# Optimization experiments

Hardware: AMD Instinct MI355X
Metric: run time of the kernel (lower is better)

## Reference

```python
import jax, jax.numpy as jnp
from jax import lax
import numpy as np

B, L, DIM = 4, 4096, 512
H, HD = 8, 64            # num_heads, head_dim
CHUNK = 128              # chunk size for chunk-recurrent lightning attention
LN_EPS = 1e-5


def _slopes(h):
    # _build_slope_tensor for power-of-2 heads: 2^(-8*(i+1)/h), cast through fp16
    s = np.array([2.0 ** (-8.0 * (i + 1) / h) for i in range(h)], dtype=np.float32)
    return jnp.asarray(s.astype(np.float16).astype(np.float32))  # [h]


def _layernorm(x, w, b):
    mu = jnp.mean(x, axis=-1, keepdims=True)
    var = jnp.mean((x - mu) ** 2, axis=-1, keepdims=True)
    return (x - mu) * lax.rsqrt(var + LN_EPS) * w + b


def _rmsnorm(x, gamma):
    # F.normalize(x, dim=-1) * sqrt(d) * gamma ; gamma [h,1,d] broadcasts over [b,h,l,d]
    n = x / jnp.maximum(jnp.linalg.norm(x, axis=-1, keepdims=True), 1e-12)
    return n * (HD ** 0.5) * gamma


def _lightning_attn(q, k, v, slopes):
    # q,k,v: [b,h,L,d]; causal linear attention with per-head decay exp(-s*(t-j))
    b, h, l, d = q.shape
    nc = l // CHUNK
    s = slopes[:, None, None]                      # [h,1,1]
    r = jnp.arange(CHUNK, dtype=q.dtype)
    diff = r[:, None] - r[None, :]                 # [C,C]
    Dintra = jnp.where(diff >= 0, jnp.exp(-s * diff), 0.0)   # [h,C,C]
    q_dec = jnp.exp(-slopes[:, None] * r[None, :])           # [h,C] decay from chunk start
    k_dec = jnp.exp(-slopes[:, None] * (CHUNK - r[None, :])) # [h,C] decay to next chunk start
    c_dec = jnp.exp(-slopes * CHUNK)                         # [h]

    def to_chunks(t):
        return t.reshape(b, h, nc, CHUNK, d).transpose(2, 0, 1, 3, 4)  # [nc,b,h,C,d]

    qc, kc, vc = to_chunks(q), to_chunks(k), to_chunks(v)

    def step(kv, inp):
        qi, ki, vi = inp                                       # [b,h,C,d]
        scores = jnp.einsum('bhid,bhjd->bhij', qi, ki) * Dintra[None]
        intra = jnp.einsum('bhij,bhjd->bhid', scores, vi)
        inter = jnp.einsum('bhcd,bhde->bhce', qi * q_dec[None, :, :, None], kv)
        kv = kv * c_dec[None, :, None, None] + jnp.einsum(
            'bhcd,bhce->bhde', ki * k_dec[None, :, :, None], vi)
        return kv, intra + inter

    kv0 = jnp.zeros((b, h, d, d), q.dtype)
    _, out = lax.scan(step, kv0, (qc, kc, vc))                 # [nc,b,h,C,d]
    return out.transpose(1, 2, 0, 3, 4).reshape(b, h, l, d)


def setup_inputs() -> dict:
    key = jax.random.key(0)
    ks = jax.random.split(key, 8)
    std = lambda fan_in: 1.0 / np.sqrt(fan_in)
    return {
        'x': jax.random.normal(ks[0], (B, L, DIM), jnp.float32),
        'ln1_w': jnp.ones((DIM,), jnp.float32),
        'ln1_b': jnp.zeros((DIM,), jnp.float32),
        'rel_bias': 0.02 * jax.random.normal(ks[1], (1, L, DIM), jnp.float32),
        'qkv_w': std(DIM) * jax.random.normal(ks[2], (3 * DIM, DIM), jnp.float32),
        'qkv_b': jnp.zeros((3 * DIM,), jnp.float32),
        'gq': jnp.ones((H, 1, HD), jnp.float32) / (HD ** 0.5),
        'gk': jnp.ones((H, 1, HD), jnp.float32) / (HD ** 0.5),
        'proj_w': std(DIM) * jax.random.normal(ks[3], (DIM, DIM), jnp.float32),
        'proj_b': jnp.zeros((DIM,), jnp.float32),
        'ln2_w': jnp.ones((DIM,), jnp.float32),
        'ln2_b': jnp.zeros((DIM,), jnp.float32),
        'fc1_w': std(DIM) * jax.random.normal(ks[4], (4 * DIM, DIM), jnp.float32),
        'fc1_b': jnp.zeros((4 * DIM,), jnp.float32),
        'fc2_w': std(4 * DIM) * jax.random.normal(ks[5], (DIM, 4 * DIM), jnp.float32),
        'fc2_b': jnp.zeros((DIM,), jnp.float32),
    }


def reference(x, ln1_w, ln1_b, rel_bias, qkv_w, qkv_b, gq, gk,
              proj_w, proj_b, ln2_w, ln2_b, fc1_w, fc1_b, fc2_w, fc2_b):
    slopes = _slopes(H)
    b, l, c = x.shape
    shortcut = x
    h = _layernorm(x, ln1_w, ln1_b)
    # --- LightningAttention ---
    h = h + rel_bias
    qkv = (h @ qkv_w.T + qkv_b).reshape(b, l, 3, H, HD).transpose(2, 0, 3, 1, 4)
    q, k, v = qkv[0], qkv[1], qkv[2]                     # [b,h,l,d]
    q = _rmsnorm(q * (HD ** -0.5), gq)
    k = _rmsnorm(k, gk)
    o = _lightning_attn(q, k, v, slopes)                 # [b,h,l,d]
    o = o.reshape(b, l, c)                               # faithful to source: reshape, no head transpose
    o = o @ proj_w.T + proj_b
    x = o + shortcut
    # --- MLP ---
    shortcut = x
    h = _layernorm(x, ln2_w, ln2_b)
    h = jax.nn.gelu(h @ fc1_w.T + fc1_b, approximate=False)
    h = h @ fc2_w.T + fc2_b
    return h + shortcut
```

## Files before the change

kernel.cpp:

```cpp
#include <hip/hip_runtime.h>
#include <math.h>

typedef unsigned short u16;
typedef __bf16 bf16x8 __attribute__((ext_vector_type(8)));
typedef float f32x4 __attribute__((ext_vector_type(4)));

#define DEVI static __device__ __forceinline__

DEVI float b2f(u16 u) { union { unsigned int i; float f; } w; w.i = ((unsigned int)u) << 16; return w.f; }
DEVI u16 f2b(float f) {
  union { float f; unsigned int i; } w; w.f = f;
  unsigned int r = (w.i + 0x7FFFu + ((w.i >> 16) & 1u)) >> 16;
  return (u16)r;
}
DEVI u16 cvt_bf16(float f) { __bf16 h = (__bf16)f; union { __bf16 h; u16 u; } w; w.h = h; return w.u; }

DEVI float fast_gelu(float v) {
  float x2 = v * v;
  float p = fmaf(0.10294357f, x2, 2.30215855f);
  float ex = exp2f(-v * p);
  return v * __builtin_amdgcn_rcpf(1.0f + ex);
}

__global__ void conv4_kernel(const float* __restrict__ s0, u16* __restrict__ d0, int n0,
                             const float* __restrict__ s1, u16* __restrict__ d1, int n1,
                             const float* __restrict__ s2, u16* __restrict__ d2, int n2,
                             const float* __restrict__ s3, u16* __restrict__ d3, int n3) {
  int i = blockIdx.x * 256 + threadIdx.x;
  int st = gridDim.x * 256;
  int tot = n0 + n1 + n2 + n3;
  for (; i < tot; i += st) {
    int j = i;
    if (j < n0) { d0[j] = f2b(s0[j]); continue; }
    j -= n0;
    if (j < n1) { d1[j] = f2b(s1[j]); continue; }
    j -= n1;
    if (j < n2) { d2[j] = f2b(s2[j]); continue; }
    j -= n2;
    d3[j] = f2b(s3[j]);
  }
}

template<int ADD_REL>
__global__ __launch_bounds__(256) void ln_kernel(
    const float* __restrict__ x, const float* __restrict__ w, const float* __restrict__ bb,
    const float* __restrict__ rel, u16* __restrict__ out) {
  int row = blockIdx.x;
  int t = threadIdx.x;
  const float* xr = x + (size_t)row * 512;
  float v0 = xr[t], v1 = xr[t + 256];
  float s = v0 + v1, ss = v0 * v0 + v1 * v1;
#pragma unroll
  for (int o = 32; o > 0; o >>= 1) { s += __shfl_down(s, o); ss += __shfl_down(ss, o); }
  __shared__ float rs[4], rss[4];
  int lane = t & 63, wid = t >> 6;
  if (lane == 0) { rs[wid] = s; rss[wid] = ss; }
  __syncthreads();
  s = rs[0] + rs[1] + rs[2] + rs[3];
  ss = rss[0] + rss[1] + rss[2] + rss[3];
  float mu = s * (1.0f / 512.0f);
  float inv = rsqrtf(ss * (1.0f / 512.0f) - mu * mu + 1e-5f);
  float o0 = (v0 - mu) * inv * w[t] + bb[t];
  float o1 = (v1 - mu) * inv * w[t + 256] + bb[t + 256];
  if (ADD_REL) {
    const float* rr = rel + (size_t)(row & 4095) * 512;
    o0 += rr[t]; o1 += rr[t + 256];
  }
  u16* orow = out + (size_t)row * 512;
  orow[t] = f2b(o0);
  orow[t + 256] = f2b(o1);
}

template<int EPI, int TM, int NSLOT>
__global__ __launch_bounds__(256) void gemm_bt_kernel(
    const u16* __restrict__ A, const u16* __restrict__ W,
    const float* __restrict__ bias, int M, int N, int K, int NBN,
    const float* __restrict__ resid, u16* __restrict__ outb,
    u16* __restrict__ q_out, u16* __restrict__ k_out, u16* __restrict__ v_out,
    float* __restrict__ outf, const float* __restrict__ gq, const float* __restrict__ gk) {
  constexpr int WM   = TM / 2;
  constexpr int NI   = TM / 32;
  constexpr int CA   = TM / 64;
  constexpr int SLOT = (TM + 128) * 32;
  __shared__ __align__(16) u16 sbuf[NSLOT * SLOT];
  int nwg = gridDim.x, wg = blockIdx.x;
  int wgs = (wg & 7) * (nwg >> 3) + (wg >> 3);
  int bn = wgs % NBN, bm = wgs / NBN;
  int m0 = bm * TM, n0 = bn * 128;
  int t = threadIdx.x, lane = t & 63, wid = t >> 6;
  int wrM = (wid >> 1) * WM, wc = (wid & 1) * 64;
  int fr = lane & 15, fq = lane >> 4;
  int srowA = wid * (TM / 4) + (lane >> 2);
  int srowB = wid * 32 + (lane >> 2);
  int scol = (((lane & 3) ^ ((lane >> 2) & 3))) * 8;
  const u16* gA = A + (size_t)(m0 + srowA) * K + scol;
  const u16* gB = W + (size_t)(n0 + srowB) * K + scol;
  f32x4 acc[NI][4] = {};
  auto AS = [&](int sel) { return &sbuf[sel * SLOT]; };
  auto BS = [&](int sel) { return &sbuf[sel * SLOT + TM * 32]; };
  auto STAGE = [&](int sel, int k0) {
    u16* lA = AS(sel) + wid * (CA * 512);
    u16* lB = BS(sel) + wid * 1024;
#pragma unroll
    for (int c = 0; c < CA; ++c)
      __builtin_amdgcn_global_load_lds(gA + k0 + c * 16 * K, lA + c * 512, 16, 0, 0);
    __builtin_amdgcn_global_load_lds(gB + k0,          lB,       16, 0, 0);
    __builtin_amdgcn_global_load_lds(gB + k0 + 16 * K, lB + 512, 16, 0, 0);
  };
  auto COMPUTE = [&](int sel) {
    bf16x8 af[NI], bfr[4];
#pragma unroll
    for (int i = 0; i < NI; ++i) {
      int ar = wrM + i * 16 + fr;
      af[i] = *(const bf16x8*)&AS(sel)[ar * 32 + ((fq ^ (ar & 3)) << 3)];
    }
#pragma unroll
    for (int j = 0; j < 4; ++j) {
      int br = wc + j * 16 + fr;
      bfr[j] = *(const bf16x8*)&BS(sel)[br * 32 + ((fq ^ (br & 3)) << 3)];
    }
#pragma unroll
    for (int i = 0; i < NI; ++i)
#pragma unroll
      for (int j = 0; j < 4; ++j)
        acc[i][j] = __builtin_amdgcn_mfma_f32_16x16x32_bf16(af[i], bfr[j], acc[i][j], 0, 0, 0);
  };
  if constexpr (NSLOT == 2) {
    STAGE(0, 0);
    asm volatile("s_waitcnt vmcnt(0)" ::: "memory");
    __builtin_amdgcn_s_barrier();
    int cur = 0;
    for (int k0 = 0; k0 < K; k0 += 32) {
      if (k0 + 32 < K) STAGE(cur ^ 1, k0 + 32);
      COMPUTE(cur);
      asm volatile("s_waitcnt vmcnt(0)" ::: "memory");
      __builtin_amdgcn_s_barrier();
      cur ^= 1;
    }
  } else {
    STAGE(0, 0);
    STAGE(1, 32);
    int cur = 0, nxt = 2;
    for (int k0 = 0; k0 < K; k0 += 32) {
      if (k0 + 32 < K) {
        if constexpr (CA == 4) { asm volatile("s_waitcnt vmcnt(6)" ::: "memory"); }
        else                   { asm volatile("s_waitcnt vmcnt(4)" ::: "memory"); }
      } else {
        asm volatile("s_waitcnt vmcnt(0)" ::: "memory");
      }
      __builtin_amdgcn_s_barrier();
      if (k0 + 64 < K) {
        STAGE(nxt, k0 + 64);
        nxt = (nxt == 2) ? 0 : nxt + 1;
      }
      COMPUTE(cur);
      cur = (cur == 2) ? 0 : cur + 1;
    }
  }
  __syncthreads();
  int fqe = lane >> 4;
  constexpr int LP = 68;
  float* lbuf = (float*)sbuf + wid * 2048;
  float bv[4];
#pragma unroll
  for (int j = 0; j < 4; ++j) bv[j] = bias[n0 + wc + j * 16 + fr];
  int rr = lane >> 2, c0 = (lane & 3) * 16;
  int nb = n0 + wc;
  int which = nb >> 9, head = (nb >> 6) & 7;
  float ggv[16];
  if (EPI == 0 && which != 2) {
    const float* gg = (which == 0) ? gq : gk;
#pragma unroll
    for (int e = 0; e < 16; ++e) ggv[e] = gg[head * 64 + c0 + e];
  }
#pragma unroll
  for (int i = 0; i < NI; ++i) {
#pragma unroll
    for (int j = 0; j < 4; ++j)
#pragma unroll
      for (int jj = 0; jj < 4; ++jj)
        lbuf[(fqe * 4 + jj) * LP + j * 16 + fr] = acc[i][j][jj] + bv[j];
    float v[16];
#pragma unroll
    for (int g = 0; g < 4; ++g) {
      f32x4 r4 = *(const f32x4*)&lbuf[rr * LP + c0 + g * 4];
#pragma unroll
      for (int e = 0; e < 4; ++e) v[g * 4 + e] = r4[e];
    }
    int gm = m0 + wrM + i * 16 + rr;
    if (EPI == 0) {
      u16* dst = (which == 0) ? q_out : (which == 1) ? k_out : v_out;
      int b = gm >> 12, l = gm & 4095;
      size_t rowbase = (((size_t)(b * 8 + head) * 4096) + l) * 64 + c0;
      union { u16 h[16]; uint4 q[2]; } pk;
      if (which == 2) {
#pragma unroll
        for (int e = 0; e < 16; ++e) pk.h[e] = cvt_bf16(v[e]);
      } else {
        float ssum = 0.f;
#pragma unroll
        for (int e = 0; e < 16; ++e) ssum += v[e] * v[e];
        ssum += __shfl_xor(ssum, 1);
        ssum += __shfl_xor(ssum, 2);
        float inv = 8.0f / fmaxf(sqrtf(ssum), 1e-12f);
#pragma unroll
        for (int e = 0; e < 16; ++e) pk.h[e] = cvt_bf16(v[e] * inv * ggv[e]);
      }
      *(uint4*)&dst[rowbase] = pk.q[0];
      *(uint4*)&dst[rowbase + 8] = pk.q[1];
    } else if (EPI == 1) {
      size_t idx = (size_t)gm * 512 + n0 + wc + c0;
#pragma unroll
      for (int g = 0; g < 4; ++g) {
        f32x4 r = *(const f32x4*)&resid[idx + g * 4];
        f32x4 o;
#pragma unroll
        for (int e = 0; e < 4; ++e) o[e] = v[g * 4 + e] + r[e];
        *(f32x4*)&outf[idx + g * 4] = o;
      }
    } else {
      union { u16 h[16]; uint4 q[2]; } pk;
#pragma unroll
      for (int e = 0; e < 16; ++e) pk.h[e] = cvt_bf16(fast_gelu(v[e]));
      size_t idx = (size_t)gm * (size_t)N + n0 + wc + c0;
      *(uint4*)&outb[idx] = pk.q[0];
      *(uint4*)&outb[idx + 8] = pk.q[1];
    }
  }
}

__global__ __launch_bounds__(256) void attn_kv_kernel(
    const u16* __restrict__ k, const u16* __restrict__ v, float* __restrict__ P) {
  constexpr int LT = 136;
  __shared__ __align__(16) u16 kT_s[64 * LT];
  __shared__ __align__(16) u16 vT_s[64 * LT];
  __shared__ float kdec[128];
  int bid = blockIdx.x;
  int bh = bid >> 5;
  float sl = exp2f(-(float)((bh & 7) + 1));
  int t = threadIdx.x, lane = t & 63, wid = t >> 6;
  for (int i = t; i < 128; i += 256) kdec[i] = expf(-sl * (float)(128 - i));
  const u16* kb = k + (size_t)bid * 8192;
  const u16* vb = v + (size_t)bid * 8192;
  __syncthreads();
  int fr = lane & 15, fk = (lane >> 4) * 8, fq = lane >> 4;
#pragma unroll
  for (int i = 0; i < 16; ++i) {
    int seg = t + i * 256;
    int j = seg >> 5, dd = (seg & 31) * 2;
    unsigned int kp = *(const unsigned int*)&kb[(size_t)j * 64 + dd];
    float kd = kdec[j];
    kT_s[dd * LT + j] = f2b(b2f((u16)(kp & 0xFFFFu)) * kd);
    kT_s[(dd + 1) * LT + j] = f2b(b2f((u16)(kp >> 16)) * kd);
    unsigned int vp = *(const unsigned int*)&vb[(size_t)j * 64 + dd];
    vT_s[dd * LT + j] = (u16)(vp & 0xFFFFu);
    vT_s[(dd + 1) * LT + j] = (u16)(vp >> 16);
  }
  __syncthreads();
  f32x4 accKV[4] = {};
#pragma unroll
  for (int kk = 0; kk < 4; ++kk) {
    bf16x8 akt = *(const bf16x8*)&kT_s[(wid * 16 + fr) * LT + kk * 32 + fk];
#pragma unroll
    for (int j = 0; j < 4; ++j) {
      bf16x8 bvt = *(const bf16x8*)&vT_s[(j * 16 + fr) * LT + kk * 32 + fk];
      accKV[j] = __builtin_amdgcn_mfma_f32_16x16x32_bf16(akt, bvt, accKV[j], 0, 0, 0);
    }
  }
  float* PT = (float*)kT_s;
  __syncthreads();
#pragma unroll
  for (int j = 0; j < 4; ++j)
#pragma unroll
    for (int jj = 0; jj < 4; ++jj) {
      int dd = wid * 16 + fq * 4 + jj;
      int e = j * 16 + fr;
      PT[e * 68 + dd] = accKV[j][jj];
    }
  __syncthreads();
  float* Pg = P + (size_t)bid * 4096;
  int e = t >> 2, d0 = (t & 3) * 16;
#pragma unroll
  for (int g = 0; g < 4; ++g) {
    f32x4 val = *(const f32x4*)&PT[e * 68 + d0 + g * 4];
    *(f32x4*)&Pg[(size_t)e * 64 + d0 + g * 4] = val;
  }
}

__global__ __launch_bounds__(256) void attn_scan_kernel(
    const float* __restrict__ P, u16* __restrict__ kvst) {
  int bh = blockIdx.x, t = threadIdx.x;
  float sl = exp2f(-(float)((bh & 7) + 1));
  float cdec = expf(-sl * 128.0f);
  float kv[16];
#pragma unroll
  for (int i = 0; i < 16; ++i) kv[i] = 0.f;
  for (int c = 0; c < 32; ++c) {
    size_t off = (((size_t)bh * 32 + c) * 4096) + (size_t)t * 16;
    union { u16 st[16]; uint4 v4[4]; } u;
#pragma unroll
    for (int i = 0; i < 16; ++i) u.st[i] = f2b(kv[i]);
    *(uint4*)&kvst[off] = u.v4[0];
    *(uint4*)&kvst[off + 8] = u.v4[1];
#pragma unroll
    for (int g = 0; g < 4; ++g) {
      f32x4 p = *(const f32x4*)&P[off + g * 4];
#pragma unroll
      for (int e = 0; e < 4; ++e) kv[g * 4 + e] = cdec * kv[g * 4 + e] + p[e];
    }
  }
}

__global__ __launch_bounds__(256) void attn_out_kernel(
    const u16* __restrict__ q, const u16* __restrict__ k, const u16* __restrict__ v,
    const u16* __restrict__ kvst, u16* __restrict__ o) {
  constexpr int LQ = 72, LT = 136, LS = 136, LKV = 72;
  __shared__ __align__(16) u16 sm[31744];
  u16* q_s  = sm;
  u16* k_s  = sm + 9216;
  u16* vT_s = sm + 18432;
  u16* kvT_s = sm + 27136;
  u16* S_s  = sm;
  __shared__ float rowf[128], colf[128];
  int bid = blockIdx.x;
  int bh = bid >> 5;
  float sl = exp2f(-(float)((bh & 7) + 1));
  int t = threadIdx.x, lane = t & 63, wid = t >> 6;
  for (int i = t; i < 128; i += 256) {
    rowf[i] = expf(-sl * i);
    colf[i] = expf(sl * i);
  }
  const u16* qb = q + (size_t)bid * 8192;
  const u16* kb = k + (size_t)bid * 8192;
  const u16* vb = v + (size_t)bid * 8192;
  const u16* kvb = kvst + (size_t)bid * 4096;
  u16* ob = o + (size_t)bid * 8192;
  int fr = lane & 15, fk = (lane >> 4) * 8, fq = lane >> 4;
#pragma unroll
  for (int i = 0; i < 4; ++i) {
    int seg = t + i * 256;
    int r = seg >> 3, cc = (seg & 7) * 8;
    *(uint4*)&q_s[r * LQ + cc] = *(const uint4*)&qb[(size_t)r * 64 + cc];
    *(uint4*)&k_s[r * LQ + cc] = *(const uint4*)&kb[(size_t)r * 64 + cc];
  }
#pragma unroll
  for (int i = 0; i < 16; ++i) {
    int seg = t + i * 256;
    int j = seg >> 5, dd = (seg & 31) * 2;
    unsigned int vp = *(const unsigned int*)&vb[(size_t)j * 64 + dd];
    vT_s[dd * LT + j] = (u16)(vp & 0xFFFFu);
    vT_s[(dd + 1) * LT + j] = (u16)(vp >> 16);
  }
#pragma unroll
  for (int i = 0; i < 2; ++i) {
    int seg = t + i * 256;
    int e = seg >> 3, dd = (seg & 7) * 8;
    *(uint4*)&kvT_s[e * LKV + dd] = *(const uint4*)&kvb[(size_t)e * 64 + dd];
  }
  __syncthreads();
  f32x4 accS[2][8] = {};
  f32x4 accI[2][4] = {};
#pragma unroll
  for (int kk = 0; kk < 2; ++kk) {
    bf16x8 aq0 = *(const bf16x8*)&q_s[(wid * 32 + fr) * LQ + kk * 32 + fk];
    bf16x8 aq1 = *(const bf16x8*)&q_s[(wid * 32 + 16 + fr) * LQ + kk * 32 + fk];
#pragma unroll
    for (int j = 0; j < 8; ++j) {
      bf16x8 bk = *(const bf16x8*)&k_s[(j * 16 + fr) * LQ + kk * 32 + fk];
      accS[0][j] = __builtin_amdgcn_mfma_f32_16x16x32_bf16(aq0, bk, accS[0][j], 0, 0, 0);
      accS[1][j] = __builtin_amdgcn_mfma_f32_16x16x32_bf16(aq1, bk, accS[1][j], 0, 0, 0);
    }
#pragma unroll
    for (int j = 0; j < 4; ++j) {
      bf16x8 bkv = *(const bf16x8*)&kvT_s[(j * 16 + fr) * LKV + kk * 32 + fk];
      accI[0][j] = __builtin_amdgcn_mfma_f32_16x16x32_bf16(aq0, bkv, accI[0][j], 0, 0, 0);
      accI[1][j] = __builtin_amdgcn_mfma_f32_16x16x32_bf16(aq1, bkv, accI[1][j], 0, 0, 0);
    }
  }
  __syncthreads();
#pragma unroll
  for (int i = 0; i < 2; ++i)
#pragma unroll
    for (int j = 0; j < 8; ++j)
#pragma unroll
      for (int jj = 0; jj < 4; ++jj) {
        int si = wid * 32 + i * 16 + fq * 4 + jj;
        int sj = j * 16 + fr;
        float val = (si >= sj) ? accS[i][j][jj] * rowf[si] * colf[sj] : 0.0f;
        S_s[si * LS + sj] = f2b(val);
      }
  __syncthreads();
  f32x4 accO[2][4] = {};
#pragma unroll
  for (int kk = 0; kk < 4; ++kk) {
    bf16x8 as0 = *(const bf16x8*)&S_s[(wid * 32 + fr) * LS + kk * 32 + fk];
    bf16x8 as1 = *(const bf16x8*)&S_s[(wid * 32 + 16 + fr) * LS + kk * 32 + fk];
#pragma unroll
    for (int j = 0; j < 4; ++j) {
      bf16x8 bvt = *(const bf16x8*)&vT_s[(j * 16 + fr) * LT + kk * 32 + fk];
      accO[0][j] = __builtin_amdgcn_mfma_f32_16x16x32_bf16(as0, bvt, accO[0][j], 0, 0, 0);
      accO[1][j] = __builtin_amdgcn_mfma_f32_16x16x32_bf16(as1, bvt, accO[1][j], 0, 0, 0);
    }
  }
#pragma unroll
  for (int i = 0; i < 2; ++i)
#pragma unroll
    for (int j = 0; j < 4; ++j)
#pragma unroll
      for (int jj = 0; jj < 4; ++jj) {
        int li = wid * 32 + i * 16 + fq * 4 + jj;
        int e = j * 16 + fr;
        float val = accO[i][j][jj] + rowf[li] * accI[i][j][jj];
        ob[(size_t)li * 64 + e] = f2b(val);
      }
}

extern "C" void kernel_launch(void* const* d_in, const int* in_sizes, int n_in,
                              void* d_out, int out_size, void* d_ws, size_t ws_size,
                              hipStream_t stream) {
  const float* x      = (const float*)d_in[0];
  const float* ln1_w  = (const float*)d_in[1];
  const float* ln1_b  = (const float*)d_in[2];
  const float* rel    = (const float*)d_in[3];
  const float* qkv_w  = (const float*)d_in[4];
  const float* qkv_b  = (const float*)d_in[5];
  const float* gq     = (const float*)d_in[6];
  const float* gk     = (const float*)d_in[7];
  const float* proj_w = (const float*)d_in[8];
  const float* proj_b = (const float*)d_in[9];
  const float* ln2_w  = (const float*)d_in[10];
  const float* ln2_b  = (const float*)d_in[11];
  const float* fc1_w  = (const float*)d_in[12];
  const float* fc1_b  = (const float*)d_in[13];
  const float* fc2_w  = (const float*)d_in[14];
  const float* fc2_b  = (const float*)d_in[15];

  char* ws = (char*)d_ws;
  size_t off = 0;
  auto alloc = [&](size_t bytes) { char* p = ws + off; off += (bytes + 255) & ~(size_t)255; return p; };
  u16* w_qkv  = (u16*)alloc((size_t)1536 * 512 * 2);
  u16* w_proj = (u16*)alloc((size_t)512 * 512 * 2);
  u16* w_fc1  = (u16*)alloc((size_t)2048 * 512 * 2);
  u16* w_fc2  = (u16*)alloc((size_t)512 * 2048 * 2);
  u16* h_buf  = (u16*)alloc((size_t)16384 * 512 * 2);
  u16* q_buf  = (u16*)alloc((size_t)8388608 * 2);
  u16* k_buf  = (u16*)alloc((size_t)8388608 * 2);
  u16* v_buf  = (u16*)alloc((size_t)8388608 * 2);
  u16* o_buf  = (u16*)alloc((size_t)8388608 * 2);
  float* x2   = (float*)alloc((size_t)8388608 * 4);
  u16* mid    = q_buf;
  float* P_glob  = x2;
  u16*   kv_state = (u16*)(x2 + 4194304);

  conv4_kernel<<<1024, 256, 0, stream>>>(qkv_w, w_qkv, 1536 * 512,
                                         proj_w, w_proj, 512 * 512,
                                         fc1_w, w_fc1, 2048 * 512,
                                         fc2_w, w_fc2, 512 * 2048);

  ln_kernel<1><<<16384, 256, 0, stream>>>(x, ln1_w, ln1_b, rel, h_buf);

  gemm_bt_kernel<0, 128, 3><<<1536, 256, 0, stream>>>(h_buf, w_qkv, qkv_b, 16384, 1536, 512, 12,
      nullptr, nullptr, q_buf, k_buf, v_buf,
      nullptr, gq, gk);

  attn_kv_kernel<<<1024, 256, 0, stream>>>(k_buf, v_buf, P_glob);
  attn_scan_kernel<<<32, 256, 0, stream>>>(P_glob, kv_state);
  attn_out_kernel<<<1024, 256, 0, stream>>>(q_buf, k_buf, v_buf, kv_state, o_buf);

  gemm_bt_kernel<1, 128, 3><<<512, 256, 0, stream>>>(o_buf, w_proj, proj_b, 16384, 512, 512, 4,
      x, nullptr, nullptr, nullptr, nullptr, x2, nullptr, nullptr);

  ln_kernel<0><<<16384, 256, 0, stream>>>(x2, ln2_w, ln2_b, nullptr, h_buf);

  gemm_bt_kernel<2, 128, 3><<<2048, 256, 0, stream>>>(h_buf, w_fc1, fc1_b, 16384, 2048, 512, 16,
      nullptr, mid, nullptr, nullptr, nullptr, nullptr, nullptr, nullptr);

  gemm_bt_kernel<1, 128, 3><<<512, 256, 0, stream>>>(mid, w_fc2, fc2_b, 16384, 512, 2048, 4,
      x2, nullptr, nullptr, nullptr, nullptr, (float*)d_out, nullptr, nullptr);

  (void)in_sizes; (void)n_in; (void)out_size; (void)ws_size;
}
```

Before: 266.4 us.

## Store residual stream and attention KV partials in bf16 instead of fp32

The intermediate residual x2, produced by the projection GEMM and consumed by the second layernorm and the final fc2 residual add, is now stored in bf16 instead of fp32. The per-chunk KV partial products passed from attn_kv to attn_scan are also stored in bf16. Both changes halve the global memory traffic for these intermediates across several kernels. The cost is reduced precision in the residual path and in the KV-state accumulation inputs, which could push the output error closer to the tolerance.

```diff
diff --git a/kernel.cpp b/kernel.cpp
--- a/kernel.cpp
+++ b/kernel.cpp
@@ -41,14 +41,20 @@
   }
 }
 
-template<int ADD_REL>
+template<int ADD_REL, int F32IN>
 __global__ __launch_bounds__(256) void ln_kernel(
-    const float* __restrict__ x, const float* __restrict__ w, const float* __restrict__ bb,
+    const void* __restrict__ xv, const float* __restrict__ w, const float* __restrict__ bb,
     const float* __restrict__ rel, u16* __restrict__ out) {
   int row = blockIdx.x;
   int t = threadIdx.x;
-  const float* xr = x + (size_t)row * 512;
-  float v0 = xr[t], v1 = xr[t + 256];
+  float v0, v1;
+  if (F32IN) {
+    const float* xr = (const float*)xv + (size_t)row * 512;
+    v0 = xr[t]; v1 = xr[t + 256];
+  } else {
+    const u16* xr = (const u16*)xv + (size_t)row * 512;
+    v0 = b2f(xr[t]); v1 = b2f(xr[t + 256]);
+  }
   float s = v0 + v1, ss = v0 * v0 + v1 * v1;
 #pragma unroll
   for (int o = 32; o > 0; o >>= 1) { s += __shfl_down(s, o); ss += __shfl_down(ss, o); }
@@ -77,7 +83,8 @@
     const float* __restrict__ bias, int M, int N, int K, int NBN,
     const float* __restrict__ resid, u16* __restrict__ outb,
     u16* __restrict__ q_out, u16* __restrict__ k_out, u16* __restrict__ v_out,
-    float* __restrict__ outf, const float* __restrict__ gq, const float* __restrict__ gk) {
+    float* __restrict__ outf, const float* __restrict__ gq, const float* __restrict__ gk,
+    const u16* __restrict__ residb) {
   constexpr int WM   = TM / 2;
   constexpr int NI   = TM / 32;
   constexpr int CA   = TM / 64;
@@ -218,19 +225,42 @@
         for (int e = 0; e < 4; ++e) o[e] = v[g * 4 + e] + r[e];
         *(f32x4*)&outf[idx + g * 4] = o;
       }
-    } else {
+    } else if (EPI == 2) {
       union { u16 h[16]; uint4 q[2]; } pk;
 #pragma unroll
       for (int e = 0; e < 16; ++e) pk.h[e] = cvt_bf16(fast_gelu(v[e]));
       size_t idx = (size_t)gm * (size_t)N + n0 + wc + c0;
       *(uint4*)&outb[idx] = pk.q[0];
       *(uint4*)&outb[idx + 8] = pk.q[1];
+    } else if (EPI == 3) {
+      size_t idx = (size_t)gm * 512 + n0 + wc + c0;
+      union { u16 h[16]; uint4 q[2]; } pk;
+#pragma unroll
+      for (int g = 0; g < 4; ++g) {
+        f32x4 r = *(const f32x4*)&resid[idx + g * 4];
+#pragma unroll
+        for (int e = 0; e < 4; ++e) pk.h[g * 4 + e] = cvt_bf16(v[g * 4 + e] + r[e]);
+      }
+      *(uint4*)&outb[idx] = pk.q[0];
+      *(uint4*)&outb[idx + 8] = pk.q[1];
+    } else {
+      size_t idx = (size_t)gm * 512 + n0 + wc + c0;
+      union { uint4 q[2]; u16 h[16]; } rb;
+      rb.q[0] = *(const uint4*)&residb[idx];
+      rb.q[1] = *(const uint4*)&residb[idx + 8];
+#pragma unroll
+      for (int g = 0; g < 4; ++g) {
+        f32x4 o;
+#pragma unroll
+        for (int e = 0; e < 4; ++e) o[e] = v[g * 4 + e] + b2f(rb.h[g * 4 + e]);
+        *(f32x4*)&outf[idx + g * 4] = o;
+      }
     }
   }
 }
 
 __global__ __launch_bounds__(256) void attn_kv_kernel(
-    const u16* __restrict__ k, const u16* __restrict__ v, float* __restrict__ P) {
+    const u16* __restrict__ k, const u16* __restrict__ v, u16* __restrict__ P) {
   constexpr int LT = 136;
   __shared__ __align__(16) u16 kT_s[64 * LT];
   __shared__ __align__(16) u16 vT_s[64 * LT];
@@ -267,7 +297,7 @@
       accKV[j] = __builtin_amdgcn_mfma_f32_16x16x32_bf16(akt, bvt, accKV[j], 0, 0, 0);
     }
   }
-  float* PT = (float*)kT_s;
+  u16* PT = kT_s;
   __syncthreads();
 #pragma unroll
   for (int j = 0; j < 4; ++j)
@@ -275,20 +305,17 @@
     for (int jj = 0; jj < 4; ++jj) {
       int dd = wid * 16 + fq * 4 + jj;
       int e = j * 16 + fr;
-      PT[e * 68 + dd] = accKV[j][jj];
-    }
-  __syncthreads();
-  float* Pg = P + (size_t)bid * 4096;
+      PT[e * 72 + dd] = cvt_bf16(accKV[j][jj]);
+    }
+  __syncthreads();
+  u16* Pg = P + (size_t)bid * 4096;
   int e = t >> 2, d0 = (t & 3) * 16;
-#pragma unroll
-  for (int g = 0; g < 4; ++g) {
-    f32x4 val = *(const f32x4*)&PT[e * 68 + d0 + g * 4];
-    *(f32x4*)&Pg[(size_t)e * 64 + d0 + g * 4] = val;
-  }
+  *(uint4*)&Pg[(size_t)e * 64 + d0]     = *(const uint4*)&PT[e * 72 + d0];
+  *(uint4*)&Pg[(size_t)e * 64 + d0 + 8] = *(const uint4*)&PT[e * 72 + d0 + 8];
 }
 
 __global__ __launch_bounds__(256) void attn_scan_kernel(
-    const float* __restrict__ P, u16* __restrict__ kvst) {
+    const u16* __restrict__ P, u16* __restrict__ kvst) {
   int bh = blockIdx.x, t = threadIdx.x;
   float sl = exp2f(-(float)((bh & 7) + 1));
   float cdec = expf(-sl * 128.0f);
@@ -297,17 +324,16 @@
   for (int i = 0; i < 16; ++i) kv[i] = 0.f;
   for (int c = 0; c < 32; ++c) {
     size_t off = (((size_t)bh * 32 + c) * 4096) + (size_t)t * 16;
-    union { u16 st[16]; uint4 v4[4]; } u;
+    union { u16 st[16]; uint4 v4[2]; } u;
 #pragma unroll
     for (int i = 0; i < 16; ++i) u.st[i] = f2b(kv[i]);
     *(uint4*)&kvst[off] = u.v4[0];
     *(uint4*)&kvst[off + 8] = u.v4[1];
-#pragma unroll
-    for (int g = 0; g < 4; ++g) {
-      f32x4 p = *(const f32x4*)&P[off + g * 4];
-#pragma unroll
-      for (int e = 0; e < 4; ++e) kv[g * 4 + e] = cdec * kv[g * 4 + e] + p[e];
-    }
+    union { uint4 q[2]; u16 h[16]; } pb;
+    pb.q[0] = *(const uint4*)&P[off];
+    pb.q[1] = *(const uint4*)&P[off + 8];
+#pragma unroll
+    for (int i = 0; i < 16; ++i) kv[i] = cdec * kv[i] + b2f(pb.h[i]);
   }
 }
 
@@ -447,36 +473,39 @@
   u16* k_buf  = (u16*)alloc((size_t)8388608 * 2);
   u16* v_buf  = (u16*)alloc((size_t)8388608 * 2);
   u16* o_buf  = (u16*)alloc((size_t)8388608 * 2);
-  float* x2   = (float*)alloc((size_t)8388608 * 4);
+  u16* x2b    = (u16*)alloc((size_t)8388608 * 2);
   u16* mid    = q_buf;
-  float* P_glob  = x2;
-  u16*   kv_state = (u16*)(x2 + 4194304);
+  u16* P_glob   = x2b;
+  u16* kv_state = x2b + 4194304;
 
   conv4_kernel<<<1024, 256, 0, stream>>>(qkv_w, w_qkv, 1536 * 512,
                                          proj_w, w_proj, 512 * 512,
                                          fc1_w, w_fc1, 2048 * 512,
                                          fc2_w, w_fc2, 512 * 2048);
 
-  ln_kernel<1><<<16384, 256, 0, stream>>>(x, ln1_w, ln1_b, rel, h_buf);
+  ln_kernel<1, 1><<<16384, 256, 0, stream>>>(x, ln1_w, ln1_b, rel, h_buf);
 
   gemm_bt_kernel<0, 128, 3><<<1536, 256, 0, stream>>>(h_buf, w_qkv, qkv_b, 16384, 1536, 512, 12,
       nullptr, nullptr, q_buf, k_buf, v_buf,
-      nullptr, gq, gk);
+      nullptr, gq, gk, nullptr);
 
   attn_kv_kernel<<<1024, 256, 0, stream>>>(k_buf, v_buf, P_glob);
   attn_scan_kernel<<<32, 256, 0, stream>>>(P_glob, kv_state);
   attn_out_kernel<<<1024, 256, 0, stream>>>(q_buf, k_buf, v_buf, kv_state, o_buf);
 
-  gemm_bt_kernel<1, 128, 3><<<512, 256, 0, stream>>>(o_buf, w_proj, proj_b, 16384, 512, 512, 4,
-      x, nullptr, nullptr, nullptr, nullptr, x2, nullptr, nullptr);
-
-  ln_kernel<0><<<16384, 256, 0, stream>>>(x2, ln2_w, ln2_b, nullptr, h_buf);
+  gemm_bt_kernel<3, 128, 3><<<512, 256, 0, stream>>>(o_buf, w_proj, proj_b, 16384, 512, 512, 4,
+      x, x2b, nullptr, nullptr, nullptr, nullptr,
+      nullptr, nullptr, nullptr);
+
+  ln_kernel<0, 0><<<16384, 256, 0, stream>>>(x2b, ln2_w, ln2_b, nullptr, h_buf);
 
   gemm_bt_kernel<2, 128, 3><<<2048, 256, 0, stream>>>(h_buf, w_fc1, fc1_b, 16384, 2048, 512, 16,
-      nullptr, mid, nullptr, nullptr, nullptr, nullptr, nullptr, nullptr);
-
-  gemm_bt_kernel<1, 128, 3><<<512, 256, 0, stream>>>(mid, w_fc2, fc2_b, 16384, 512, 2048, 4,
-      x2, nullptr, nullptr, nullptr, nullptr, (float*)d_out, nullptr, nullptr);
+      nullptr, mid, nullptr, nullptr, nullptr, nullptr,
+      nullptr, nullptr, nullptr);
+
+  gemm_bt_kernel<4, 128, 3><<<512, 256, 0, stream>>>(mid, w_fc2, fc2_b, 16384, 512, 2048, 4,
+      nullptr, nullptr, nullptr, nullptr, nullptr, (float*)d_out,
+      nullptr, nullptr, x2b);
 
   (void)in_sizes; (void)n_in; (void)out_size; (void)ws_size;
 }
```

New measurement: 255.8 us (median of 2 runs). 4.0% less time.
